# Optimization experiments

Measured on AMD Instinct MI355X. Metric: run time of the kernel, lower is better.

The kernel has to match this reference:

```python
import jax, jax.numpy as jnp
import numpy as np

B, Nq, C = 1, 40000, 256
Hh, L, P = 8, 4, 8
hd = C // Hh
LEVEL_SHAPES = [(128, 128), (64, 64), (32, 32), (16, 16)]


def setup_inputs() -> dict:
    key = jax.random.key(0)
    ks = jax.random.split(key, 16)
    inp = {}
    inp['query'] = jax.random.normal(ks[0], (B, Nq, C), jnp.float32)
    # reference points in [-1, 1] normalized coords (x, y)
    inp['reference_points'] = jax.random.uniform(ks[1], (B, Nq, L, 2), jnp.float32) * 2.0 - 1.0
    for i, (h, w) in enumerate(LEVEL_SHAPES):
        inp[f'feat{i}'] = jax.random.normal(ks[2 + i], (B, C, h, w), jnp.float32)
    # learned params (torch Linear y = x @ W + b, W stored as [in, out])
    inp['W_off'] = jax.random.normal(ks[6], (C, Hh * L * P * 2), jnp.float32) * 0.02
    inp['b_off'] = jax.random.normal(ks[7], (Hh * L * P * 2,), jnp.float32) * 0.5
    inp['W_attn'] = jax.random.normal(ks[8], (C, Hh * L * P), jnp.float32) * 0.02
    inp['b_attn'] = jnp.zeros((Hh * L * P,), jnp.float32)
    inp['W_val'] = jax.random.normal(ks[9], (C, C), jnp.float32) * (1.0 / np.sqrt(C))
    inp['b_val'] = jnp.zeros((C,), jnp.float32)
    inp['W_out'] = jax.random.normal(ks[10], (C, C), jnp.float32) * (1.0 / np.sqrt(C))
    inp['b_out'] = jnp.zeros((C,), jnp.float32)
    return inp


def _deform_sample(v, coords):
    # Bilinear grid_sample, align_corners=True, zeros padding.
    # v: [B, Hh, H, W, hd]; coords: [B, Hh, S, 2] in [-1, 1] (x, y)
    _, _, H, W, _ = v.shape
    x = (coords[..., 0] + 1.0) * 0.5 * (W - 1)
    y = (coords[..., 1] + 1.0) * 0.5 * (H - 1)
    x0 = jnp.floor(x)
    y0 = jnp.floor(y)
    vflat = v.reshape(v.shape[0], v.shape[1], H * W, v.shape[4])

    def corner(xi, yi, w):
        inb = (xi >= 0) & (xi <= W - 1) & (yi >= 0) & (yi <= H - 1)
        idx = (jnp.clip(yi, 0, H - 1) * W + jnp.clip(xi, 0, W - 1)).astype(jnp.int32)
        g = jnp.take_along_axis(vflat, idx[..., None], axis=2)  # [B,Hh,S,hd]
        return g * (w * inb)[..., None]

    return (corner(x0, y0, (x0 + 1 - x) * (y0 + 1 - y))
            + corner(x0 + 1, y0, (x - x0) * (y0 + 1 - y))
            + corner(x0, y0 + 1, (x0 + 1 - x) * (y - y0))
            + corner(x0 + 1, y0 + 1, (x - x0) * (y - y0)))


def reference(query, feat0, feat1, feat2, feat3, reference_points,
              W_off, b_off, W_attn, b_attn, W_val, b_val, W_out, b_out):
    feats = [feat0, feat1, feat2, feat3]
    off = (query @ W_off + b_off).reshape(B, Nq, Hh, L, P, 2)
    w = (query @ W_attn + b_attn).reshape(B, Nq, Hh, L, P)
    w = jax.nn.softmax(w, axis=-1)  # softmax over points, per level
    # samp: [B, Nq, Hh, L, P, 2]
    samp = reference_points[:, :, None, :, None, :] + jnp.tanh(off) * 0.25

    out = jnp.zeros((B, Nq, Hh, hd), jnp.float32)
    for l, f in enumerate(feats):
        Hl, Wl = f.shape[2], f.shape[3]
        v = jnp.einsum('bchw,cd->bhwd', f, W_val) + b_val  # value proj
        v = v.reshape(B, Hl, Wl, Hh, hd).transpose(0, 3, 1, 2, 4)  # [B,Hh,H,W,hd]
        coords = samp[:, :, :, l].transpose(0, 2, 1, 3, 4).reshape(B, Hh, Nq * P, 2)
        s = _deform_sample(v, coords).reshape(B, Hh, Nq, P, hd)
        wl = w[:, :, :, l].transpose(0, 2, 1, 3)  # [B,Hh,Nq,P]
        out = out + jnp.einsum('bhnpd,bhnp->bnhd', s, wl)

    return out.reshape(B, Nq, C) @ W_out + b_out
```

## Files before the change

### kernel.cpp

```cpp
#include <hip/hip_runtime.h>
#include <hip/hip_fp16.h>
#include <math.h>

#define NQ 40000

typedef short s16x8 __attribute__((ext_vector_type(8)));
typedef float f32x4 __attribute__((ext_vector_type(4)));

static constexpr int HLa[4] = {128, 64, 32, 16};
static constexpr int HWa[4] = {16384, 4096, 1024, 256};
static constexpr int VB[4] = {0, 4194304, 5242880, 5505024};

__device__ __forceinline__ short bf16hi(float x) {
    union { float f; unsigned u; } v; v.f = x;
    unsigned r = v.u + 0x7FFFu + ((v.u >> 16) & 1u);
    return (short)(r >> 16);
}
__device__ __forceinline__ float bf16f(short s) {
    union { unsigned u; float f; } v; v.u = ((unsigned)(unsigned short)s) << 16;
    return v.f;
}
__device__ __forceinline__ float fast_tanh(float x) {
    float xc = fminf(fmaxf(x, -15.f), 15.f);
    float e = __expf(2.f * xc);
    return (e - 1.f) / (e + 1.f);
}
#define MFMA16(a, b, c) __builtin_amdgcn_mfma_f32_16x16x32_bf16(a, b, c, 0, 0, 0)

__global__ __launch_bounds__(256) void prep_w(
    const float* __restrict__ Woff, const float* __restrict__ Wattn,
    const float* __restrict__ Wout, short* __restrict__ WtH, short* __restrict__ WtL)
{
    int r = blockIdx.x, c = threadIdx.x;
    float x;
    if (r < 512)      x = Woff[c * 512 + r];
    else if (r < 768) x = Wattn[c * 256 + (r - 512)];
    else              x = Wout[c * 256 + (r - 768)];
    short hi = bf16hi(x);
    WtH[r * 256 + c] = hi;
    WtL[r * 256 + c] = bf16hi(x - bf16f(hi));
}

__global__ __launch_bounds__(256) void vproj_kernel(
    const float* __restrict__ f0, const float* __restrict__ f1,
    const float* __restrict__ f2, const float* __restrict__ f3,
    const float* __restrict__ Wv, const float* __restrict__ bv,
    __half* __restrict__ v)
{
    __shared__ float fT[256 * 16];

    int bid = blockIdx.x;
    const float* f;
    int base, HWl, hw0;
    if (bid < 1024)      { f = f0; base = VB[0]; HWl = 16384; hw0 = bid * 16; }
    else if (bid < 1280) { f = f1; base = VB[1]; HWl = 4096;  hw0 = (bid - 1024) * 16; }
    else if (bid < 1344) { f = f2; base = VB[2]; HWl = 1024;  hw0 = (bid - 1280) * 16; }
    else                 { f = f3; base = VB[3]; HWl = 256;   hw0 = (bid - 1344) * 16; }

    int t = threadIdx.x;
    for (int k = 0; k < 16; ++k) {
        int idx = k * 256 + t;
        int c = idx >> 4, j = idx & 15;
        fT[idx] = f[c * HWl + hw0 + j];
    }
    __syncthreads();

    int to4 = (t & 63) * 4;
    int hw4 = (t >> 6) * 4;

    float4 bv4 = *(const float4*)(bv + to4);
    float acc[4][4];
    #pragma unroll
    for (int i = 0; i < 4; ++i) {
        acc[i][0] = bv4.x; acc[i][1] = bv4.y; acc[i][2] = bv4.z; acc[i][3] = bv4.w;
    }

    #pragma unroll 4
    for (int c = 0; c < 256; ++c) {
        float4 w4 = *(const float4*)(Wv + c * 256 + to4);
        float4 fv = *(const float4*)(fT + c * 16 + hw4);
        float fa[4] = {fv.x, fv.y, fv.z, fv.w};
        float wa[4] = {w4.x, w4.y, w4.z, w4.w};
        #pragma unroll
        for (int i = 0; i < 4; ++i)
            #pragma unroll
            for (int j = 0; j < 4; ++j)
                acc[i][j] += fa[i] * wa[j];
    }

    int hh = to4 >> 5, dd4 = to4 & 31;
    #pragma unroll
    for (int i = 0; i < 4; ++i) {
        int hw = hw0 + hw4 + i;
        __half2 h0 = __floats2half2_rn(acc[i][0], acc[i][1]);
        __half2 h1 = __floats2half2_rn(acc[i][2], acc[i][3]);
        uint2 st = make_uint2(*(unsigned*)&h0, *(unsigned*)&h1);
        *(uint2*)(v + base + (hh * HWl + hw) * 32 + dd4) = st;
    }
}

__global__ __launch_bounds__(256, 4) void msda_hp_kernel(
    const float* __restrict__ query, const float* __restrict__ refp,
    const float* __restrict__ boff,  const float* __restrict__ battn,
    const short* __restrict__ WtH,   const short* __restrict__ WtL,
    const __half* __restrict__ v,    __half* __restrict__ preTg)
{
    __shared__ __align__(16) char lds[30720];
    __half* sWh = (__half*)(lds + 16896);
    float*  sR  = (float*)(lds + 28672);

    const int t = threadIdx.x;
    const int hp = blockIdx.x & 3;
    const int n0 = (blockIdx.x >> 2) * 64;
    const int wv = t >> 6, lane = t & 63;
    const int mrow = lane & 15, kg = lane >> 4;
    float*    offW = (float*)lds + wv * 1056;
    unsigned* sPIw = (unsigned*)(lds + 25600 + wv * 768);
    uint2*    sPWw = (uint2*)(lds + 25600 + wv * 768 + 256);

    sR[t]       = refp[n0 * 8 + t];
    sR[t + 256] = refp[n0 * 8 + t + 256];
    __syncthreads();

    f32x4 accO[8], accA[4];
    {
        f32x4 z = {0.f, 0.f, 0.f, 0.f};
        #pragma unroll
        for (int j = 0; j < 8; ++j) accO[j] = z;
        #pragma unroll
        for (int j = 0; j < 4; ++j) accA[j] = z;
    }
    {
        const float* qrow = query + (n0 + wv * 16 + mrow) * 256 + kg * 8;
        const short* offH = WtH + (hp * 128 + mrow) * 256 + kg * 8;
        const short* offLo = WtL + (hp * 128 + mrow) * 256 + kg * 8;
        const short* attH = WtH + (512 + hp * 64 + mrow) * 256 + kg * 8;
        const short* attL = WtL + (512 + hp * 64 + mrow) * 256 + kg * 8;
        #pragma unroll
        for (int kk = 0; kk < 8; ++kk) {
            float4 qa = *(const float4*)(qrow + kk * 32);
            float4 qb = *(const float4*)(qrow + kk * 32 + 4);
            float qv[8] = {qa.x, qa.y, qa.z, qa.w, qb.x, qb.y, qb.z, qb.w};
            s16x8 ah, al;
            #pragma unroll
            for (int e = 0; e < 8; ++e) {
                short hi = bf16hi(qv[e]);
                ah[e] = hi;
                al[e] = bf16hi(qv[e] - bf16f(hi));
            }
            #pragma unroll
            for (int j = 0; j < 8; ++j) {
                s16x8 bh = *(const s16x8*)(offH + j * 4096 + kk * 32);
                s16x8 bl = *(const s16x8*)(offLo + j * 4096 + kk * 32);
                accO[j] = MFMA16(ah, bh, accO[j]);
                accO[j] = MFMA16(al, bh, accO[j]);
                accO[j] = MFMA16(ah, bl, accO[j]);
            }
            #pragma unroll
            for (int ja = 0; ja < 4; ++ja) {
                s16x8 bh = *(const s16x8*)(attH + ja * 4096 + kk * 32);
                s16x8 bl = *(const s16x8*)(attL + ja * 4096 + kk * 32);
                accA[ja] = MFMA16(ah, bh, accA[ja]);
                accA[ja] = MFMA16(al, bh, accA[ja]);
                accA[ja] = MFMA16(ah, bl, accA[ja]);
            }
        }
    }
    #pragma unroll
    for (int j = 0; j < 8; ++j) {
        float bb = boff[hp * 128 + j * 16 + mrow];
        #pragma unroll
        for (int r = 0; r < 4; ++r) accO[j][r] += bb;
    }
    #pragma unroll
    for (int ja = 0; ja < 4; ++ja) {
        float bb = battn[hp * 64 + ja * 16 + mrow];
        #pragma unroll
        for (int r = 0; r < 4; ++r) accA[ja][r] += bb;
    }

    #pragma unroll
    for (int ja = 0; ja < 4; ++ja) {
        int hhL = ja >> 1;
        int l   = ((ja & 1) << 1) | (mrow >> 3);
        int p   = mrow & 7;
        #pragma unroll
        for (int r = 0; r < 4; ++r) {
            float x = accA[ja][r];
            float m = fmaxf(x, __shfl_xor(x, 1));
            m = fmaxf(m, __shfl_xor(m, 2));
            m = fmaxf(m, __shfl_xor(m, 4));
            float e = __expf(x - m);
            float s = e + __shfl_xor(e, 1);
            s += __shfl_xor(s, 2);
            s += __shfl_xor(s, 4);
            int ql = wv * 16 + kg * 4 + r;
            sWh[ql * 68 + hhL * 32 + l * 8 + p] = __float2half_rn(e / s);
        }
    }

    const int l_p = (lane >> 3) & 3;
    const int Wl_p = 128 >> l_p;
    const float scl_p = 0.5f * (float)(Wl_p - 1);
    const int sg = kg, ch2 = mrow;
    const int Wl_s = 128 >> sg;
    const int HWs = Wl_s * Wl_s;
    const int dyoMul = Wl_s * 16;
    const int VBs = (sg == 0) ? VB[0] : (sg == 1) ? VB[1] : (sg == 2) ? VB[2] : VB[3];
    const __half2* vl0 = (const __half2*)(v + VBs + (2 * hp) * HWs * 32) + ch2;
    const __half2* vl1 = (const __half2*)(v + VBs + (2 * hp + 1) * HWs * 32) + ch2;

    for (int sp = 0; sp < 2; ++sp) {
        if ((kg >> 1) == sp) {
            #pragma unroll
            for (int j = 0; j < 8; ++j)
                #pragma unroll
                for (int r = 0; r < 4; ++r)
                    offW[((kg & 1) * 4 + r) * 132 + j * 16 + mrow] = accO[j][r];
        }

        for (int c8 = 0; c8 < 8; ++c8) {
            const int chunk = sp * 8 + c8;
            const int ql = wv * 16 + chunk;
            {
                float2 ll = *(const float2*)(offW + c8 * 132 + 2 * lane);
                float lx = ll.x, ly = ll.y;
                float w  = __half2float(sWh[ql * 68 + lane]);
                float rx = sR[ql * 8 + l_p * 2], ry = sR[ql * 8 + l_p * 2 + 1];
                float cx = rx + fast_tanh(lx) * 0.25f;
                float cy = ry + fast_tanh(ly) * 0.25f;
                float xx = (cx + 1.f) * scl_p, yy = (cy + 1.f) * scl_p;
                float x0f = floorf(xx), y0f = floorf(yy);
                float fx = xx - x0f, fy = yy - y0f;
                int x0 = (int)x0f, y0 = (int)y0f;
                int xc0 = min(max(x0, 0), Wl_p - 1);
                int xc1 = min(max(x0 + 1, 0), Wl_p - 1);
                int yc0 = min(max(y0, 0), Wl_p - 1);
                int yc1 = min(max(y0 + 1, 0), Wl_p - 1);
                bool bx0 = (x0 >= 0) & (x0 < Wl_p);
                bool bx1 = (x0 + 1 >= 0) & (x0 + 1 < Wl_p);
                bool by0 = (y0 >= 0) & (y0 < Wl_p);
                bool by1 = (y0 + 1 >= 0) & (y0 + 1 < Wl_p);
                float w00 = (bx0 && by0) ? (1.f - fx) * (1.f - fy) * w : 0.f;
                float w01 = (bx1 && by0) ? fx * (1.f - fy) * w : 0.f;
                float w10 = (bx0 && by1) ? (1.f - fx) * fy * w : 0.f;
                float w11 = (bx1 && by1) ? fx * fy * w : 0.f;
                unsigned pw = (unsigned)(yc0 * Wl_p + xc0)
                            | ((unsigned)(xc1 - xc0) << 14)
                            | ((unsigned)(yc1 - yc0) << 15);
                sPIw[lane] = pw;
                __half2 hA = __floats2half2_rn(w00, w01);
                __half2 hB = __floats2half2_rn(w10, w11);
                sPWw[lane] = make_uint2(*(unsigned*)&hA, *(unsigned*)&hB);
            }

            #pragma unroll
            for (int hhL = 0; hhL < 2; ++hhL) {
                const __half2* vl = hhL ? vl1 : vl0;
                unsigned gw0[8], gw1[8], gw2[8], gw3[8];
                uint2 wwv[8];
                #pragma unroll
                for (int p = 0; p < 8; ++p) {
                    int rec = hhL * 32 + sg * 8 + p;
                    unsigned pw = sPIw[rec];
                    wwv[p] = sPWw[rec];
                    int idx = pw & 0x3FFF;
                    int dxo = ((pw >> 14) & 1) * 16;
                    int dyo = ((pw >> 15) & 1) * dyoMul;
                    const __half2* b00 = vl + idx * 16;
                    gw0[p] = *(const unsigned*)(b00);
                    gw1[p] = *(const unsigned*)(b00 + dxo);
                    gw2[p] = *(const unsigned*)(b00 + dyo);
                    gw3[p] = *(const unsigned*)(b00 + dxo + dyo);
                }
                __builtin_amdgcn_sched_barrier(0);
                float ax = 0.f, ay = 0.f;
                #pragma unroll
                for (int p = 0; p < 8; ++p) {
                    float2 fa = __half22float2(*(__half2*)&wwv[p].x);
                    float2 fb = __half22float2(*(__half2*)&wwv[p].y);
                    float2 f00 = __half22float2(*(__half2*)&gw0[p]);
                    float2 f01 = __half22float2(*(__half2*)&gw1[p]);
                    float2 f10 = __half22float2(*(__half2*)&gw2[p]);
                    float2 f11 = __half22float2(*(__half2*)&gw3[p]);
                    ax += fa.x * f00.x + fa.y * f01.x + fb.x * f10.x + fb.y * f11.x;
                    ay += fa.x * f00.y + fa.y * f01.y + fb.x * f10.y + fb.y * f11.y;
                }
                float sxv = ax + __shfl_xor(ax, 16); sxv += __shfl_xor(sxv, 32);
                float syv = ay + __shfl_xor(ay, 16); syv += __shfl_xor(syv, 32);
                if (sg == 0)
                    *(__half2*)(preTg + (n0 + ql) * 256 + (2 * hp + hhL) * 32 + ch2 * 2) =
                        __floats2half2_rn(sxv, syv);
            }
        }
    }
}

__global__ __launch_bounds__(256, 4) void outproj_kernel(
    const __half* __restrict__ preTg, const short* __restrict__ WtH,
    const short* __restrict__ WtL,    const float* __restrict__ bout,
    float* __restrict__ out)
{
    __shared__ __align__(16) char lds[16896];
    short* sQh = (short*)lds;
    short* sQl = (short*)(lds + 8448);

    const int t = threadIdx.x;
    const int n0 = blockIdx.x * 16;
    const int wv = t >> 6, lane = t & 63;
    const int mrow = lane & 15, kg = lane >> 4;

    {
        int q = t >> 4, seg = t & 15;
        const uint2* src = (const uint2*)(preTg + (n0 + q) * 256 + seg * 16);
        short* dh = sQh + q * 264 + seg * 16;
        short* dl = sQl + q * 264 + seg * 16;
        #pragma unroll
        for (int jj = 0; jj < 4; ++jj) {
            uint2 u = src[jj];
            float2 fA = __half22float2(*(__half2*)&u.x);
            float2 fB = __half22float2(*(__half2*)&u.y);
            short h0 = bf16hi(fA.x), h1 = bf16hi(fA.y);
            short h2 = bf16hi(fB.x), h3 = bf16hi(fB.y);
            dh[4 * jj]     = h0;
            dh[4 * jj + 1] = h1;
            dh[4 * jj + 2] = h2;
            dh[4 * jj + 3] = h3;
            dl[4 * jj]     = bf16hi(fA.x - bf16f(h0));
            dl[4 * jj + 1] = bf16hi(fA.y - bf16f(h1));
            dl[4 * jj + 2] = bf16hi(fB.x - bf16f(h2));
            dl[4 * jj + 3] = bf16hi(fB.y - bf16f(h3));
        }
    }
    __syncthreads();

    f32x4 accE[4];
    f32x4 z = {0.f, 0.f, 0.f, 0.f};
    #pragma unroll
    for (int e = 0; e < 4; ++e) accE[e] = z;
    const short* outH = WtH + (768 + wv * 64 + mrow) * 256 + kg * 8;
    const short* outL = WtL + (768 + wv * 64 + mrow) * 256 + kg * 8;
    const int aoff = mrow * 264 + kg * 8;
    #pragma unroll
    for (int kk = 0; kk < 8; ++kk) {
        s16x8 ah = *(const s16x8*)(sQh + aoff + kk * 32);
        s16x8 al = *(const s16x8*)(sQl + aoff + kk * 32);
        #pragma unroll
        for (int e = 0; e < 4; ++e) {
            s16x8 bh = *(const s16x8*)(outH + e * 4096 + kk * 32);
            s16x8 bl = *(const s16x8*)(outL + e * 4096 + kk * 32);
            accE[e] = MFMA16(ah, bh, accE[e]);
            accE[e] = MFMA16(al, bh, accE[e]);
            accE[e] = MFMA16(ah, bl, accE[e]);
        }
    }
    #pragma unroll
    for (int e = 0; e < 4; ++e) {
        int col = wv * 64 + e * 16 + mrow;
        float bb = bout[col];
        #pragma unroll
        for (int r = 0; r < 4; ++r)
            out[(n0 + kg * 4 + r) * 256 + col] = accE[e][r] + bb;
    }
}

extern "C" void kernel_launch(void* const* d_in, const int* in_sizes, int n_in,
                              void* d_out, int out_size, void* d_ws, size_t ws_size,
                              hipStream_t stream) {
    const float* query = (const float*)d_in[0];
    const float* refp  = (const float*)d_in[1];
    const float* f0    = (const float*)d_in[2];
    const float* f1    = (const float*)d_in[3];
    const float* f2    = (const float*)d_in[4];
    const float* f3    = (const float*)d_in[5];
    const float* Woff  = (const float*)d_in[6];
    const float* boff  = (const float*)d_in[7];
    const float* Wattn = (const float*)d_in[8];
    const float* battn = (const float*)d_in[9];
    const float* Wval  = (const float*)d_in[10];
    const float* bval  = (const float*)d_in[11];
    const float* Wout  = (const float*)d_in[12];
    const float* bout  = (const float*)d_in[13];

    char* ws = (char*)d_ws;
    __half* v  = (__half*)ws;
    short* WtH = (short*)(ws + 11141120);
    short* WtL = (short*)(ws + 11665408);
    __half* preTg = (__half*)(ws + 12189696);
    float* outp = (float*)d_out;

    prep_w<<<1024, 256, 0, stream>>>(Woff, Wattn, Wout, WtH, WtL);
    vproj_kernel<<<1360, 256, 0, stream>>>(f0, f1, f2, f3, Wval, bval, v);
    msda_hp_kernel<<<2500, 256, 0, stream>>>(query, refp, boff, battn,
                                             WtH, WtL, v, preTg);
    outproj_kernel<<<2500, 256, 0, stream>>>(preTg, WtH, WtL, bout, outp);
}
```

Before: 535.4 us.

## Shrink sampling kernel to single-wave blocks and drop explicit gather batching

The deformable-sampling kernel is now launched as 10000 one-wavefront blocks of 16 queries, where it used to run 2500 four-wave blocks. Each block now holds only its own LDS slice and no longer needs the block-wide barrier after loading reference points. The explicit batching of the 32 gather loads before a sched_barrier is also removed, so the compiler is free to interleave the loads with the FMAs. The aim is lower LDS and register pressure, more resident waves, and no barrier. The risk is less memory-level parallelism per wave and more per-block setup repeated across four times as many blocks.

Measured after the change: 547.0 us. +2.2%, slower.

```diff
diff --git a/kernel.cpp b/kernel.cpp
--- a/kernel.cpp
+++ b/kernel.cpp
@@ -99,28 +99,26 @@
     }
 }
 
-__global__ __launch_bounds__(256, 4) void msda_hp_kernel(
+__global__ __launch_bounds__(64, 8) void msda_hp_kernel(
     const float* __restrict__ query, const float* __restrict__ refp,
     const float* __restrict__ boff,  const float* __restrict__ battn,
     const short* __restrict__ WtH,   const short* __restrict__ WtL,
     const __half* __restrict__ v,    __half* __restrict__ preTg)
 {
-    __shared__ __align__(16) char lds[30720];
-    __half* sWh = (__half*)(lds + 16896);
-    float*  sR  = (float*)(lds + 28672);
-
-    const int t = threadIdx.x;
+    __shared__ __align__(16) char lds[7680];
+    float*    offW = (float*)lds;
+    __half*   sWh  = (__half*)(lds + 4224);
+    unsigned* sPIw = (unsigned*)(lds + 6400);
+    uint2*    sPWw = (uint2*)(lds + 6656);
+    float*    sR   = (float*)(lds + 7168);
+
+    const int lane = threadIdx.x;
     const int hp = blockIdx.x & 3;
-    const int n0 = (blockIdx.x >> 2) * 64;
-    const int wv = t >> 6, lane = t & 63;
+    const int n0 = (blockIdx.x >> 2) * 16;
     const int mrow = lane & 15, kg = lane >> 4;
-    float*    offW = (float*)lds + wv * 1056;
-    unsigned* sPIw = (unsigned*)(lds + 25600 + wv * 768);
-    uint2*    sPWw = (uint2*)(lds + 25600 + wv * 768 + 256);
-
-    sR[t]       = refp[n0 * 8 + t];
-    sR[t + 256] = refp[n0 * 8 + t + 256];
-    __syncthreads();
+
+    sR[lane]      = refp[n0 * 8 + lane];
+    sR[lane + 64] = refp[n0 * 8 + 64 + lane];
 
     f32x4 accO[8], accA[4];
     {
@@ -131,7 +129,7 @@
         for (int j = 0; j < 4; ++j) accA[j] = z;
     }
     {
-        const float* qrow = query + (n0 + wv * 16 + mrow) * 256 + kg * 8;
+        const float* qrow = query + (n0 + mrow) * 256 + kg * 8;
         const short* offH = WtH + (hp * 128 + mrow) * 256 + kg * 8;
         const short* offLo = WtL + (hp * 128 + mrow) * 256 + kg * 8;
         const short* attH = WtH + (512 + hp * 64 + mrow) * 256 + kg * 8;
@@ -194,7 +192,7 @@
             float s = e + __shfl_xor(e, 1);
             s += __shfl_xor(s, 2);
             s += __shfl_xor(s, 4);
-            int ql = wv * 16 + kg * 4 + r;
+            int ql = kg * 4 + r;
             sWh[ql * 68 + hhL * 32 + l * 8 + p] = __float2half_rn(e / s);
         }
     }
@@ -220,8 +218,7 @@
         }
 
         for (int c8 = 0; c8 < 8; ++c8) {
-            const int chunk = sp * 8 + c8;
-            const int ql = wv * 16 + chunk;
+            const int ql = sp * 8 + c8;
             {
                 float2 ll = *(const float2*)(offW + c8 * 132 + 2 * lane);
                 float lx = ll.x, ly = ll.y;
@@ -257,32 +254,22 @@
             #pragma unroll
             for (int hhL = 0; hhL < 2; ++hhL) {
                 const __half2* vl = hhL ? vl1 : vl0;
-                unsigned gw0[8], gw1[8], gw2[8], gw3[8];
-                uint2 wwv[8];
+                float ax = 0.f, ay = 0.f;
                 #pragma unroll
                 for (int p = 0; p < 8; ++p) {
                     int rec = hhL * 32 + sg * 8 + p;
                     unsigned pw = sPIw[rec];
-                    wwv[p] = sPWw[rec];
+                    uint2 ww = sPWw[rec];
                     int idx = pw & 0x3FFF;
                     int dxo = ((pw >> 14) & 1) * 16;
                     int dyo = ((pw >> 15) & 1) * dyoMul;
                     const __half2* b00 = vl + idx * 16;
-                    gw0[p] = *(const unsigned*)(b00);
-                    gw1[p] = *(const unsigned*)(b00 + dxo);
-                    gw2[p] = *(const unsigned*)(b00 + dyo);
-                    gw3[p] = *(const unsigned*)(b00 + dxo + dyo);
-                }
-                __builtin_amdgcn_sched_barrier(0);
-                float ax = 0.f, ay = 0.f;
-                #pragma unroll
-                for (int p = 0; p < 8; ++p) {
-                    float2 fa = __half22float2(*(__half2*)&wwv[p].x);
-                    float2 fb = __half22float2(*(__half2*)&wwv[p].y);
-                    float2 f00 = __half22float2(*(__half2*)&gw0[p]);
-                    float2 f01 = __half22float2(*(__half2*)&gw1[p]);
-                    float2 f10 = __half22float2(*(__half2*)&gw2[p]);
-                    float2 f11 = __half22float2(*(__half2*)&gw3[p]);
+                    float2 fa = __half22float2(*(__half2*)&ww.x);
+                    float2 fb = __half22float2(*(__half2*)&ww.y);
+                    float2 f00 = __half22float2(b00[0]);
+                    float2 f01 = __half22float2(b00[dxo]);
+                    float2 f10 = __half22float2(b00[dyo]);
+                    float2 f11 = __half22float2(b00[dxo + dyo]);
                     ax += fa.x * f00.x + fa.y * f01.x + fb.x * f10.x + fb.y * f11.x;
                     ay += fa.x * f00.y + fa.y * f01.y + fb.x * f10.y + fb.y * f11.y;
                 }
@@ -391,7 +378,7 @@
 
     prep_w<<<1024, 256, 0, stream>>>(Woff, Wattn, Wout, WtH, WtL);
     vproj_kernel<<<1360, 256, 0, stream>>>(f0, f1, f2, f3, Wval, bval, v);
-    msda_hp_kernel<<<2500, 256, 0, stream>>>(query, refp, boff, battn,
+    msda_hp_kernel<<<10000, 64, 0, stream>>>(query, refp, boff, battn,
                                              WtH, WtL, v, preTg);
     outproj_kernel<<<2500, 256, 0, stream>>>(preTg, WtH, WtL, bout, outp);
 }
```
